# Kernel optimization log

Measured on AMD Instinct MI355X. Metric: run time of the kernel, lower is better.

Reference implementation:

```python
import jax, jax.numpy as jnp
import numpy as np

HIDDEN = 2048
N_HEADS = 16
N_KV = 4
HEAD_DIM = 128
SEQ = 2048
BATCH = 2
THETA = 10000.0


def rotate_half(x):
    half = x.shape[-1] // 2
    x1, x2 = x[..., :half], x[..., half:]
    return jnp.concatenate((-x2, x1), axis=-1)


def rope_cos_sin(seq_len, dim, theta, dtype):
    inv_freq = 1.0 / (theta ** (jnp.arange(0, dim, 2, dtype=jnp.float32) / dim))
    t = jnp.arange(seq_len, dtype=jnp.float32)
    freqs = jnp.einsum('i,j->ij', t, inv_freq)            # [S, dim/2]
    emb = jnp.concatenate((freqs, freqs), axis=-1)        # [S, dim]
    return jnp.cos(emb).astype(dtype), jnp.sin(emb).astype(dtype)


def setup_inputs() -> dict:
    key = jax.random.key(0)
    kx, kq, kk, kv, ko = jax.random.split(key, 5)
    s = 0.02
    return {
        'x':  jax.random.normal(kx, (BATCH, SEQ, HIDDEN), dtype=jnp.float32),
        'Wq': jax.random.normal(kq, (HIDDEN, N_HEADS * HEAD_DIM), dtype=jnp.float32) * s,
        'Wk': jax.random.normal(kk, (HIDDEN, N_KV * HEAD_DIM), dtype=jnp.float32) * s,
        'Wv': jax.random.normal(kv, (HIDDEN, N_KV * HEAD_DIM), dtype=jnp.float32) * s,
        'Wo': jax.random.normal(ko, (N_HEADS * HEAD_DIM, HIDDEN), dtype=jnp.float32) * s,
    }


def reference(x, Wq, Wk, Wv, Wo):
    B, S, _ = x.shape
    q = (x @ Wq).reshape(B, S, N_HEADS, HEAD_DIM)
    k = (x @ Wk).reshape(B, S, N_KV, HEAD_DIM)
    v = (x @ Wv).reshape(B, S, N_KV, HEAD_DIM)

    cos, sin = rope_cos_sin(S, HEAD_DIM, THETA, x.dtype)
    cos = cos[None, :, None, :]  # [1,S,1,D]
    sin = sin[None, :, None, :]
    q = q * cos + rotate_half(q) * sin
    k = k * cos + rotate_half(k) * sin

    repeat = N_HEADS // N_KV
    k = jnp.repeat(k, repeat, axis=2)  # repeat_interleave over heads
    v = jnp.repeat(v, repeat, axis=2)

    # [B,H,S,D]
    q = q.transpose(0, 2, 1, 3)
    k = k.transpose(0, 2, 1, 3)
    v = v.transpose(0, 2, 1, 3)

    scale = HEAD_DIM ** -0.5
    scores = jnp.einsum('bhqd,bhkd->bhqk', q, k) * scale
    causal = jnp.triu(jnp.full((S, S), -jnp.inf, dtype=scores.dtype), k=1)
    scores = scores + causal
    probs = jax.nn.softmax(scores, axis=-1)
    out = jnp.einsum('bhqk,bhkd->bhqd', probs, v)
    out = out.transpose(0, 2, 1, 3).reshape(B, S, N_HEADS * HEAD_DIM)
    return out @ Wo
```

## Files before the change

kernel.cpp:

```cpp
#include <hip/hip_runtime.h>
#include <hip/hip_bf16.h>
#include <math.h>

#define HIDDEN 2048
#define NHEADS 16
#define NKV 4
#define HD 128
#define SEQ 2048
#define BATCH 2
#define MTOT (BATCH*SEQ)
#define NQ (NHEADS*HD)
#define NKVD (NKV*HD)
#define NQKV (NQ + 2*NKVD)

typedef __attribute__((ext_vector_type(8))) short short8;
typedef __attribute__((ext_vector_type(4))) float float4v;

#if __has_builtin(__builtin_amdgcn_exp2f)
#define EXP2F __builtin_amdgcn_exp2f
#else
#define EXP2F exp2f
#endif
#define C1 0.1275174f

static __device__ __forceinline__ unsigned short f2bf(float f) {
  union { float f; unsigned int u; } v; v.f = f;
  unsigned int r = v.u + 0x7FFF + ((v.u >> 16) & 1);
  return (unsigned short)(r >> 16);
}
static __device__ __forceinline__ float bf2f(unsigned short h) {
  union { unsigned int u; float f; } v; v.u = ((unsigned int)h) << 16;
  return v.f;
}

static __device__ __forceinline__ void async16(const unsigned short* g, unsigned short* l) {
  __builtin_amdgcn_global_load_lds(
      (const __attribute__((address_space(1))) unsigned int*)g,
      (__attribute__((address_space(3))) unsigned int*)l, 16, 0, 0);
}

__global__ void cast_f32_bf16(const float* __restrict__ in,
                              unsigned short* __restrict__ out, int n) {
  int i = (blockIdx.x * blockDim.x + threadIdx.x) * 4;
  if (i < n) {
    float4 v = *(const float4*)(in + i);
    ushort4 o;
    o.x = f2bf(v.x); o.y = f2bf(v.y); o.z = f2bf(v.z); o.w = f2bf(v.w);
    *(ushort4*)(out + i) = o;
  }
}

__global__ void transpose_cast(const float* __restrict__ W,
                               unsigned short* __restrict__ Wt, int K, int N) {
  __shared__ float tile[32][33];
  int tn = blockIdx.x * 32;
  int tk = blockIdx.y * 32;
  int tx = threadIdx.x & 31;
  int ty = threadIdx.x >> 5;
  #pragma unroll
  for (int i = 0; i < 4; i++) {
    int k = tk + ty + i * 8;
    tile[ty + i * 8][tx] = W[(size_t)k * N + tn + tx];
  }
  __syncthreads();
  #pragma unroll
  for (int i = 0; i < 4; i++) {
    int n = tn + ty + i * 8;
    Wt[(size_t)n * K + tk + tx] = f2bf(tile[tx][ty + i * 8]);
  }
}

__global__ void rope_kernel(unsigned short* __restrict__ Qb, int nheads) {
  int idx = blockIdx.x * blockDim.x + threadIdx.x;
  int d = idx & 63;
  int hr = idx >> 6;
  int spos = (hr / nheads) % SEQ;
  size_t base = (size_t)hr * HD;
  float inv = exp2f((float)d * -0.2076205059304601f);
  float ang = (float)spos * inv;
  float sn, cs;
  sincosf(ang, &sn, &cs);
  float q1 = bf2f(Qb[base + d]);
  float q2 = bf2f(Qb[base + d + 64]);
  Qb[base + d]      = f2bf(q1 * cs - q2 * sn);
  Qb[base + d + 64] = f2bf(q2 * cs + q1 * sn);
}

__global__ __launch_bounds__(512, 2) void gemm_qkv(
    const unsigned short* __restrict__ A,
    const unsigned short* __restrict__ Bt,
    unsigned short* __restrict__ Qb,
    unsigned short* __restrict__ Kb,
    unsigned short* __restrict__ Vt) {
  __shared__ __align__(16) unsigned short L[4 * 16384];
  const int K = HIDDEN;
  const int NT = K / 32;
  int bm = blockIdx.y * 256, bn = blockIdx.x * 256;
  int tid = threadIdx.x, w = tid >> 6, lane = tid & 63;
  int wrow = w >> 2, wcol = w & 3;
  int m16 = lane & 15, quad = lane >> 4;
  int lrow = lane >> 2, lch = lane & 3;
  int lchs = lch ^ ((lrow >> 1) & 3);
  int qx = quad ^ ((m16 >> 1) & 3);
  const unsigned short* Ag = A + (size_t)(bm + w * 32 + lrow) * K + lchs * 8;
  const unsigned short* Bg = Bt + (size_t)(bn + w * 32 + lrow) * K + lchs * 8;

  float4v acc[8][4];
  #pragma unroll
  for (int i = 0; i < 8; i++)
    #pragma unroll
    for (int j = 0; j < 4; j++) acc[i][j] = (float4v)0.0f;

  auto stage = [&](int t) {
    unsigned short* Lb = L + (t & 3) * 16384;
    int k0 = t * 32;
    #pragma unroll
    for (int i = 0; i < 2; i++) {
      async16(Ag + (size_t)i * 16 * K + k0, Lb + w * 1024 + i * 512);
      async16(Bg + (size_t)i * 16 * K + k0, Lb + 8192 + w * 1024 + i * 512);
    }
  };

  const bool isV = (blockIdx.x >= 10);

  stage(0); stage(1);
  asm volatile("s_waitcnt vmcnt(4)" ::: "memory");
  __builtin_amdgcn_s_barrier();
  __builtin_amdgcn_sched_barrier(0);

  if (!isV) {
    for (int t = 0; t < NT; ++t) {
      if (t + 2 < NT) stage(t + 2);
      const unsigned short* Ab_ = L + (t & 3) * 16384;
      const unsigned short* Bb_ = Ab_ + 8192;
      short8 af[8], bfr[4];
      #pragma unroll
      for (int i = 0; i < 8; i++)
        af[i] = *(const short8*)(&Ab_[(wrow * 128 + i * 16 + m16) * 32 + qx * 8]);
      #pragma unroll
      for (int j = 0; j < 4; j++)
        bfr[j] = *(const short8*)(&Bb_[(wcol * 64 + j * 16 + m16) * 32 + qx * 8]);
      __builtin_amdgcn_s_setprio(1);
      #pragma unroll
      for (int i = 0; i < 8; i++)
        #pragma unroll
        for (int j = 0; j < 4; j++)
          acc[i][j] = __builtin_amdgcn_mfma_f32_16x16x32_bf16(af[i], bfr[j], acc[i][j], 0, 0, 0);
      __builtin_amdgcn_s_setprio(0);
      if (t + 2 < NT) { asm volatile("s_waitcnt vmcnt(4)" ::: "memory"); }
      else            { asm volatile("s_waitcnt vmcnt(0)" ::: "memory"); }
      __builtin_amdgcn_s_barrier();
      __builtin_amdgcn_sched_barrier(0);
    }
  } else {
    for (int t = 0; t < NT; ++t) {
      if (t + 2 < NT) stage(t + 2);
      const unsigned short* Ab_ = L + (t & 3) * 16384;
      const unsigned short* Bb_ = Ab_ + 8192;
      short8 af[8], bfr[4];
      #pragma unroll
      for (int i = 0; i < 8; i++)
        af[i] = *(const short8*)(&Ab_[(wrow * 128 + i * 16 + m16) * 32 + qx * 8]);
      #pragma unroll
      for (int j = 0; j < 4; j++)
        bfr[j] = *(const short8*)(&Bb_[(wcol * 64 + j * 16 + m16) * 32 + qx * 8]);
      __builtin_amdgcn_s_setprio(1);
      #pragma unroll
      for (int i = 0; i < 8; i++)
        #pragma unroll
        for (int j = 0; j < 4; j++)
          acc[i][j] = __builtin_amdgcn_mfma_f32_16x16x32_bf16(bfr[j], af[i], acc[i][j], 0, 0, 0);
      __builtin_amdgcn_s_setprio(0);
      if (t + 2 < NT) { asm volatile("s_waitcnt vmcnt(4)" ::: "memory"); }
      else            { asm volatile("s_waitcnt vmcnt(0)" ::: "memory"); }
      __builtin_amdgcn_s_barrier();
      __builtin_amdgcn_sched_barrier(0);
    }
  }

  if (blockIdx.x < 8) {
    #pragma unroll
    for (int i = 0; i < 8; i++)
      #pragma unroll
      for (int j = 0; j < 4; j++)
        #pragma unroll
        for (int r = 0; r < 4; r++) {
          int row = bm + wrow * 128 + i * 16 + quad * 4 + r;
          int col = bn + wcol * 64 + j * 16 + m16;
          Qb[(size_t)row * NQ + col] = f2bf(acc[i][j][r]);
        }
  } else if (!isV) {
    #pragma unroll
    for (int i = 0; i < 8; i++)
      #pragma unroll
      for (int j = 0; j < 4; j++)
        #pragma unroll
        for (int r = 0; r < 4; r++) {
          int row = bm + wrow * 128 + i * 16 + quad * 4 + r;
          int col = bn - 2048 + wcol * 64 + j * 16 + m16;
          Kb[(size_t)row * NKVD + col] = f2bf(acc[i][j][r]);
        }
  } else {
    #pragma unroll
    for (int i = 0; i < 8; i++)
      #pragma unroll
      for (int j = 0; j < 4; j++)
        #pragma unroll
        for (int r = 0; r < 4; r++) {
          int f = bn - 2560 + wcol * 64 + j * 16 + quad * 4 + r;
          int m = bm + wrow * 128 + i * 16 + m16;
          Vt[(size_t)f * MTOT + m] = f2bf(acc[i][j][r]);
        }
  }
}

__global__ __launch_bounds__(256) void gemm_o(
    const unsigned short* __restrict__ A,
    const unsigned short* __restrict__ Bt,
    float* __restrict__ C, int M, int N, int K) {
  __shared__ unsigned short As0[128 * 32], Bs0[128 * 32];
  __shared__ unsigned short As1[128 * 32], Bs1[128 * 32];
  int bm = blockIdx.y * 128, bn = blockIdx.x * 128;
  int tid = threadIdx.x, w = tid >> 6, lane = tid & 63;
  int wm = (w >> 1) * 64, wn = (w & 1) * 64;
  int m16 = lane & 15, quad = lane >> 4;
  int lrow = lane >> 2, lch = lane & 3;
  int lchs = lch ^ ((lrow >> 1) & 3);
  int qx = quad ^ ((m16 >> 1) & 3);
  const unsigned short* Ag = A + (size_t)(bm + w * 32 + lrow) * K + lchs * 8;
  const unsigned short* Bg = Bt + (size_t)(bn + w * 32 + lrow) * K + lchs * 8;
  int woff = w * 1024;

  float4v acc[4][4];
  #pragma unroll
  for (int i = 0; i < 4; i++)
    #pragma unroll
    for (int j = 0; j < 4; j++) acc[i][j] = (float4v)0.0f;

  auto stage = [&](int k0, unsigned short* Asl, unsigned short* Bsl) {
    #pragma unroll
    for (int i = 0; i < 2; i++) {
      async16(Ag + (size_t)i * 16 * K + k0, Asl + woff + i * 512);
      async16(Bg + (size_t)i * 16 * K + k0, Bsl + woff + i * 512);
    }
  };
  auto compute = [&](const unsigned short* As, const unsigned short* Bs) {
    short8 af[4], bfr[4];
    #pragma unroll
    for (int i = 0; i < 4; i++)
      af[i] = *(const short8*)(&As[(wm + i * 16 + m16) * 32 + qx * 8]);
    #pragma unroll
    for (int j = 0; j < 4; j++)
      bfr[j] = *(const short8*)(&Bs[(wn + j * 16 + m16) * 32 + qx * 8]);
    #pragma unroll
    for (int i = 0; i < 4; i++)
      #pragma unroll
      for (int j = 0; j < 4; j++)
        acc[i][j] = __builtin_amdgcn_mfma_f32_16x16x32_bf16(af[i], bfr[j], acc[i][j], 0, 0, 0);
  };

  stage(0, As0, Bs0);
  for (int k0 = 0; k0 < K; k0 += 64) {
    __syncthreads();
    if (k0 + 32 < K) stage(k0 + 32, As1, Bs1);
    compute(As0, Bs0);
    __syncthreads();
    if (k0 + 64 < K) stage(k0 + 64, As0, Bs0);
    compute(As1, Bs1);
  }

  #pragma unroll
  for (int i = 0; i < 4; i++)
    #pragma unroll
    for (int j = 0; j < 4; j++)
      #pragma unroll
      for (int r = 0; r < 4; r++) {
        int row = bm + wm + i * 16 + quad * 4 + r;
        int col = bn + wn + j * 16 + m16;
        C[(size_t)row * N + col] = acc[i][j][r];
      }
}

#define FLASH_TILE(CUR, NXT)                                                  \
  {                                                                           \
    const int ktb = kt * 64;                                                  \
    __syncthreads();        \
    {                                                                         \
      const unsigned short* Vg = Vt + vgrow * (size_t)MTOT                    \
                                    + (size_t)b * SEQ + ktb + kcv * 32 + vlch * 8; \
      unsigned short* Vl = Vs + kcv * 4096 + ipv * 512;                       \
      _Pragma("unroll")                                                       \
      for (int i = 0; i < 4; i++) async16(Vg + (size_t)i * 16 * MTOT, Vl + i * 512); \
    }                                                                         \
    if (kt < H) {                                                             \
      const unsigned short* Kg = Kp + (((size_t)b * SEQ + (kt + 1) * 64 + lrow) * NKV + kvh) * HD + w * 32 + vlch * 8; \
      unsigned short* Kl = NXT + w * 2048;                                    \
      _Pragma("unroll")                                                       \
      for (int i = 0; i < 4; i++) async16(Kg + (size_t)i * 16 * NKV * HD, Kl + i * 512); \
    }                                                                         \
    const bool act1 = (ktb <= lmax_w);                                        \
    float4v sacc[2][4];                                                       \
    _Pragma("unroll") for (int s4 = 0; s4 < 4; s4++) {                        \
      sacc[0][s4] = (float4v)0.0f; sacc[1][s4] = (float4v)0.0f; }             \
    __builtin_amdgcn_s_setprio(1);                                            \
    if (act1) {                                                               \
      _Pragma("unroll")                                                       \
      for (int s4 = 0; s4 < 4; s4++)                                          \
        _Pragma("unroll")                                                     \
        for (int c = 0; c < 4; c++) {                                         \
          short8 kf = *(const short8*)(&CUR[c * 2048 + (s4 * 16 + m16) * 32 + qx * 8]); \
          sacc[0][s4] = __builtin_amdgcn_mfma_f32_16x16x32_bf16(kf, qf[0][c], sacc[0][s4], 0, 0, 0); \
          sacc[1][s4] = __builtin_amdgcn_mfma_f32_16x16x32_bf16(kf, qf[1][c], sacc[1][s4], 0, 0, 0); \
        }                                                                     \
    } else {                                                                  \
      _Pragma("unroll")                                                       \
      for (int s4 = 0; s4 < 4; s4++)                                          \
        _Pragma("unroll")                                                     \
        for (int c = 0; c < 4; c++) {                                         \
          short8 kf = *(const short8*)(&CUR[c * 2048 + (s4 * 16 + m16) * 32 + qx * 8]); \
          sacc[0][s4] = __builtin_amdgcn_mfma_f32_16x16x32_bf16(kf, qf[0][c], sacc[0][s4], 0, 0, 0); \
        }                                                                     \
    }                                                                         \
    __builtin_amdgcn_s_setprio(0);                                            \
    _Pragma("unroll")                                                         \
    for (int qs = 0; qs < 2; qs++) {                                          \
      if (qs == 0 || act1) {                                                  \
        const int tb = qs ? L : H;                                            \
        const int qabs = tb * 64 + w * 16 + m16;                              \
        const bool diag = (kt == tb);                                         \
        float sv[4][4]; float mloc = -1e30f;                                  \
        if (diag) {                                                           \
          _Pragma("unroll") for (int s4 = 0; s4 < 4; s4++)                    \
            _Pragma("unroll") for (int r = 0; r < 4; r++) {                   \
              int kabs = ktb + s4 * 16 + quad * 4 + r;                        \
              float t = sacc[qs][s4][r];                                      \
              sv[s4][r] = (kabs > qabs) ? -1e30f : t;                         \
              mloc = fmaxf(mloc, sv[s4][r]); }                                \
        } else {                                                              \
          _Pragma("unroll") for (int s4 = 0; s4 < 4; s4++)                    \
            _Pragma("unroll") for (int r = 0; r < 4; r++) {                   \
              sv[s4][r] = sacc[qs][s4][r]; mloc = fmaxf(mloc, sv[s4][r]); }   \
        }                                                                     \
        mloc *= C1;                                                           \
        mloc = fmaxf(mloc, __shfl_xor(mloc, 16, 64));                         \
        mloc = fmaxf(mloc, __shfl_xor(mloc, 32, 64));                         \
        float mnewS = fmaxf(miS[qs], mloc);                                   \
        const bool defer = (bool)__all(mloc <= miS[qs] + 8.0f);               \
        if (defer) mnewS = miS[qs];  \
        const int prow = qs * 64 + w * 16 + m16;                              \
        const int psw = prow * 32; const int rx = prow & 7;                   \
        float rs = 0.0f;                                                      \
        _Pragma("unroll") for (int s4 = 0; s4 < 4; s4++) {                    \
          float p0 = EXP2F(__builtin_fmaf(sv[s4][0], C1, -mnewS));            \
          float p1 = EXP2F(__builtin_fmaf(sv[s4][1], C1, -mnewS));            \
          float p2 = EXP2F(__builtin_fmaf(sv[s4][2], C1, -mnewS));            \
          float p3 = EXP2F(__builtin_fmaf(sv[s4][3], C1, -mnewS));            \
          rs += p0 + p1 + p2 + p3;                                            \
          uint2 u;                                                            \
          u.x = (__float_as_uint(p1) & 0xffff0000u) | (__float_as_uint(p0) >> 16); \
          u.y = (__float_as_uint(p3) & 0xffff0000u) | (__float_as_uint(p2) >> 16); \
          int chunkW = s4 * 2 + (quad >> 1);                                  \
          *(uint2*)(&Ps[psw + ((chunkW ^ rx) << 2) + (quad & 1) * 2]) = u;    \
        }                                                                     \
        rs += __shfl_xor(rs, 16, 64);                                         \
        rs += __shfl_xor(rs, 32, 64);                                         \
        if (!defer) {                                                         \
          const float alpha = EXP2F(miS[qs] - mnewS);                         \
          li[qs] *= alpha; miS[qs] = mnewS;                                   \
          _Pragma("unroll") for (int ds = 0; ds < 8; ds++) oacc[ds][qs] *= alpha; \
        }                                                                     \
        li[qs] += rs;                                                         \
      }                                                                       \
    }                                                                         \
    __syncthreads();     \
    {                                                                         \
      const int r0 = w * 16 + m16, r1 = 64 + w * 16 + m16;                    \
      __builtin_amdgcn_s_setprio(1);                                          \
      if (act1) {                                                             \
        _Pragma("unroll")                                                     \
        for (int kc = 0; kc < 2; kc++) {                                      \
          short8 pf0 = *(const short8*)(&Ps[r0 * 32 + (((kc * 4 + quad) ^ (r0 & 7)) << 2)]); \
          short8 pf1 = *(const short8*)(&Ps[r1 * 32 + (((kc * 4 + quad) ^ (r1 & 7)) << 2)]); \
          _Pragma("unroll")                                                   \
          for (int ds = 0; ds < 8; ds++) {                                    \
            short8 vf = *(const short8*)(&Vs[kc * 4096 + (ds * 16 + m16) * 32 + qx * 8]); \
            oacc[ds][0] = __builtin_amdgcn_mfma_f32_16x16x32_bf16(vf, pf0, oacc[ds][0], 0, 0, 0); \
            oacc[ds][1] = __builtin_amdgcn_mfma_f32_16x16x32_bf16(vf, pf1, oacc[ds][1], 0, 0, 0); \
          }                                                                   \
        }                                                                     \
      } else {                                                                \
        _Pragma("unroll")                                                     \
        for (int kc = 0; kc < 2; kc++) {                                      \
          short8 pf0 = *(const short8*)(&Ps[r0 * 32 + (((kc * 4 + quad) ^ (r0 & 7)) << 2)]); \
          _Pragma("unroll")                                                   \
          for (int ds = 0; ds < 8; ds++) {                                    \
            short8 vf = *(const short8*)(&Vs[kc * 4096 + (ds * 16 + m16) * 32 + qx * 8]); \
            oacc[ds][0] = __builtin_amdgcn_mfma_f32_16x16x32_bf16(vf, pf0, oacc[ds][0], 0, 0, 0); \
          }                                                                   \
        }                                                                     \
      }                                                                       \
      __builtin_amdgcn_s_setprio(0);                                          \
    }                                                                         \
  }

__global__ __launch_bounds__(256, 2) void flash_attn(
    const unsigned short* __restrict__ Q,
    const unsigned short* __restrict__ Kp,
    const unsigned short* __restrict__ Vt,
    unsigned short* __restrict__ O) {
  __shared__ unsigned short Ks0[4 * 64 * 32];
  __shared__ unsigned short Ks1[4 * 64 * 32];
  __shared__ unsigned short Vs[2 * 128 * 32];
  __shared__ unsigned int   Ps[128 * 32];

  int bx = blockIdx.x;
  int h  = blockIdx.y;
  int b  = blockIdx.z;
  int kvh = h >> 2;
  int H = 31 - bx, L = bx;
  int tid = threadIdx.x;
  int w = tid >> 6, lane = tid & 63;
  int m16 = lane & 15, quad = lane >> 4;
  int lrow = lane >> 2, lch = lane & 3;
  const int vlch = lch ^ ((lrow >> 1) & 3);
  const int qx = quad ^ ((m16 >> 1) & 3);
  const int lmax_w = L * 64 + w * 16 + 15;

  const int kcv = w >> 1, ipv = (w & 1) * 4;
  const size_t vgrow = (size_t)kvh * HD + ipv * 16 + lrow;

  short8 qf[2][4];
  #pragma unroll
  for (int qs = 0; qs < 2; qs++) {
    int tb = qs ? L : H;
    size_t qbase = (((size_t)b * SEQ + tb * 64 + w * 16 + m16) * NHEADS + h) * HD;
    #pragma unroll
    for (int c = 0; c < 4; c++)
      qf[qs][c] = *(const short8*)(Q + qbase + c * 32 + quad * 8);
  }

  float4v oacc[8][2];
  #pragma unroll
  for (int ds = 0; ds < 8; ds++) { oacc[ds][0] = (float4v)0.0f; oacc[ds][1] = (float4v)0.0f; }
  float miS[2] = {-1e30f, -1e30f}, li[2] = {0.0f, 0.0f};

  {
    const unsigned short* Kg = Kp + (((size_t)b * SEQ + lrow) * NKV + kvh) * HD + w * 32 + vlch * 8;
    unsigned short* Kl = Ks0 + w * 2048;
    #pragma unroll
    for (int i = 0; i < 4; i++) async16(Kg + (size_t)i * 16 * NKV * HD, Kl + i * 512);
  }

  int kt = 0;
  for (;;) {
    FLASH_TILE(Ks0, Ks1)
    if (++kt > H) break;
    FLASH_TILE(Ks1, Ks0)
    if (++kt > H) break;
  }

  #pragma unroll
  for (int qs = 0; qs < 2; qs++) {
    float inv = 1.0f / li[qs];
    int tb = qs ? L : H;
    int qabs = tb * 64 + w * 16 + m16;
    size_t obase = (((size_t)b * SEQ + qabs) * NHEADS + h) * HD + quad * 4;
    #pragma unroll
    for (int ds = 0; ds < 8; ds++) {
      float v0 = oacc[ds][qs][0] * inv;
      float v1 = oacc[ds][qs][1] * inv;
      float v2 = oacc[ds][qs][2] * inv;
      float v3 = oacc[ds][qs][3] * inv;
      uint2 u;
      u.x = ((unsigned)f2bf(v1) << 16) | f2bf(v0);
      u.y = ((unsigned)f2bf(v3) << 16) | f2bf(v2);
      *(uint2*)(O + obase + ds * 16) = u;
    }
  }
}

extern "C" void kernel_launch(void* const* d_in, const int* in_sizes, int n_in,
                              void* d_out, int out_size, void* d_ws, size_t ws_size,
                              hipStream_t stream) {
  const float* x  = (const float*)d_in[0];
  const float* Wq = (const float*)d_in[1];
  const float* Wk = (const float*)d_in[2];
  const float* Wv = (const float*)d_in[3];
  const float* Wo = (const float*)d_in[4];
  float* out = (float*)d_out;

  unsigned short* ws = (unsigned short*)d_ws;
  unsigned short* xb  = ws;
  unsigned short* Wqt = xb  + (size_t)MTOT * HIDDEN;
  unsigned short* Wkt = Wqt + (size_t)NQ * HIDDEN;
  unsigned short* Wvt = Wkt + (size_t)NKVD * HIDDEN;
  unsigned short* Wot = Wvt + (size_t)NKVD * HIDDEN;
  unsigned short* Qb  = Wot + (size_t)NQ * HIDDEN;
  unsigned short* Kb  = Qb  + (size_t)MTOT * NQ;
  unsigned short* Vtb = Kb  + (size_t)MTOT * NKVD;
  unsigned short* Ab  = Vtb + (size_t)MTOT * NKVD;

  cast_f32_bf16<<<(MTOT * HIDDEN / 4 + 255) / 256, 256, 0, stream>>>(x, xb, MTOT * HIDDEN);
  transpose_cast<<<dim3(NQ / 32, HIDDEN / 32), 256, 0, stream>>>(Wq, Wqt, HIDDEN, NQ);
  transpose_cast<<<dim3(NKVD / 32, HIDDEN / 32), 256, 0, stream>>>(Wk, Wkt, HIDDEN, NKVD);
  transpose_cast<<<dim3(NKVD / 32, HIDDEN / 32), 256, 0, stream>>>(Wv, Wvt, HIDDEN, NKVD);
  transpose_cast<<<dim3(NQ / 32, HIDDEN / 32), 256, 0, stream>>>(Wo, Wot, NQ, HIDDEN);

  gemm_qkv<<<dim3(NQKV / 256, MTOT / 256), 512, 0, stream>>>(xb, Wqt, Qb, Kb, Vtb);

  rope_kernel<<<(BATCH * SEQ * NHEADS * 64) / 256, 256, 0, stream>>>(Qb, NHEADS);
  rope_kernel<<<(BATCH * SEQ * NKV * 64) / 256, 256, 0, stream>>>(Kb, NKV);

  flash_attn<<<dim3(16, NHEADS, BATCH), 256, 0, stream>>>(Qb, Kb, Vtb, Ab);

  gemm_o<<<dim3(HIDDEN / 128, MTOT / 128), 256, 0, stream>>>(Ab, Wot, out, MTOT, HIDDEN, NQ);
}
```

Baseline: 300.3 us.

## Deepen GEMM prefetch to three stages and double-buffer V tiles in flash attention

```diff
diff --git a/kernel.cpp b/kernel.cpp
--- a/kernel.cpp
+++ b/kernel.cpp
@@ -123,14 +123,14 @@
 
   const bool isV = (blockIdx.x >= 10);
 
-  stage(0); stage(1);
-  asm volatile("s_waitcnt vmcnt(4)" ::: "memory");
+  stage(0); stage(1); stage(2);
+  asm volatile("s_waitcnt vmcnt(8)" ::: "memory");
   __builtin_amdgcn_s_barrier();
   __builtin_amdgcn_sched_barrier(0);
 
   if (!isV) {
     for (int t = 0; t < NT; ++t) {
-      if (t + 2 < NT) stage(t + 2);
+      if (t + 3 < NT) stage(t + 3);
       const unsigned short* Ab_ = L + (t & 3) * 16384;
       const unsigned short* Bb_ = Ab_ + 8192;
       short8 af[8], bfr[4];
@@ -147,14 +147,15 @@
         for (int j = 0; j < 4; j++)
           acc[i][j] = __builtin_amdgcn_mfma_f32_16x16x32_bf16(af[i], bfr[j], acc[i][j], 0, 0, 0);
       __builtin_amdgcn_s_setprio(0);
-      if (t + 2 < NT) { asm volatile("s_waitcnt vmcnt(4)" ::: "memory"); }
-      else            { asm volatile("s_waitcnt vmcnt(0)" ::: "memory"); }
+      if (t + 3 < NT)      { asm volatile("s_waitcnt vmcnt(8)" ::: "memory"); }
+      else if (t + 2 < NT) { asm volatile("s_waitcnt vmcnt(4)" ::: "memory"); }
+      else                 { asm volatile("s_waitcnt vmcnt(0)" ::: "memory"); }
       __builtin_amdgcn_s_barrier();
       __builtin_amdgcn_sched_barrier(0);
     }
   } else {
     for (int t = 0; t < NT; ++t) {
-      if (t + 2 < NT) stage(t + 2);
+      if (t + 3 < NT) stage(t + 3);
       const unsigned short* Ab_ = L + (t & 3) * 16384;
       const unsigned short* Bb_ = Ab_ + 8192;
       short8 af[8], bfr[4];
@@ -171,8 +172,9 @@
         for (int j = 0; j < 4; j++)
           acc[i][j] = __builtin_amdgcn_mfma_f32_16x16x32_bf16(bfr[j], af[i], acc[i][j], 0, 0, 0);
       __builtin_amdgcn_s_setprio(0);
-      if (t + 2 < NT) { asm volatile("s_waitcnt vmcnt(4)" ::: "memory"); }
-      else            { asm volatile("s_waitcnt vmcnt(0)" ::: "memory"); }
+      if (t + 3 < NT)      { asm volatile("s_waitcnt vmcnt(8)" ::: "memory"); }
+      else if (t + 2 < NT) { asm volatile("s_waitcnt vmcnt(4)" ::: "memory"); }
+      else                 { asm volatile("s_waitcnt vmcnt(0)" ::: "memory"); }
       __builtin_amdgcn_s_barrier();
       __builtin_amdgcn_sched_barrier(0);
     }
@@ -281,23 +283,28 @@
       }
 }
 
-#define FLASH_TILE(CUR, NXT)                                                  \
+#define FLASH_TILE(CUR, NXT, PC, PN)                                          \
   {                                                                           \
     const int ktb = kt * 64;                                                  \
-    __syncthreads();        \
-    {                                                                         \
+    asm volatile("s_waitcnt lgkmcnt(0)" ::: "memory");                        \
+    __builtin_amdgcn_s_barrier();             \
+    __builtin_amdgcn_sched_barrier(0);                                        \
+    if (kt < H) {                                                             \
       const unsigned short* Vg = Vt + vgrow * (size_t)MTOT                    \
-                                    + (size_t)b * SEQ + ktb + kcv * 32 + vlch * 8; \
-      unsigned short* Vl = Vs + kcv * 4096 + ipv * 512;                       \
+                                    + (size_t)b * SEQ + (ktb + 64) + kcv * 32 + vlch * 8; \
+      unsigned short* Vl = Vs + (PN) * 8192 + kcv * 4096 + ipv * 512;         \
       _Pragma("unroll")                                                       \
       for (int i = 0; i < 4; i++) async16(Vg + (size_t)i * 16 * MTOT, Vl + i * 512); \
-    }                                                                         \
-    if (kt < H) {                                                             \
       const unsigned short* Kg = Kp + (((size_t)b * SEQ + (kt + 1) * 64 + lrow) * NKV + kvh) * HD + w * 32 + vlch * 8; \
       unsigned short* Kl = NXT + w * 2048;                                    \
       _Pragma("unroll")                                                       \
       for (int i = 0; i < 4; i++) async16(Kg + (size_t)i * 16 * NKV * HD, Kl + i * 512); \
+      asm volatile("s_waitcnt vmcnt(8)" ::: "memory");                        \
+    } else {                                                                  \
+      asm volatile("s_waitcnt vmcnt(0)" ::: "memory");                        \
     }                                                                         \
+    __builtin_amdgcn_s_barrier();       \
+    __builtin_amdgcn_sched_barrier(0);                                        \
     const bool act1 = (ktb <= lmax_w);                                        \
     float4v sacc[2][4];                                                       \
     _Pragma("unroll") for (int s4 = 0; s4 < 4; s4++) {                        \
@@ -372,7 +379,8 @@
         li[qs] += rs;                                                         \
       }                                                                       \
     }                                                                         \
-    __syncthreads();     \
+    asm volatile("s_waitcnt lgkmcnt(0)" ::: "memory");  \
+    __builtin_amdgcn_sched_barrier(0);                                        \
     {                                                                         \
       const int r0 = w * 16 + m16, r1 = 64 + w * 16 + m16;                    \
       __builtin_amdgcn_s_setprio(1);                                          \
@@ -383,7 +391,7 @@
           short8 pf1 = *(const short8*)(&Ps[r1 * 32 + (((kc * 4 + quad) ^ (r1 & 7)) << 2)]); \
           _Pragma("unroll")                                                   \
           for (int ds = 0; ds < 8; ds++) {                                    \
-            short8 vf = *(const short8*)(&Vs[kc * 4096 + (ds * 16 + m16) * 32 + qx * 8]); \
+            short8 vf = *(const short8*)(&Vs[(PC) * 8192 + kc * 4096 + (ds * 16 + m16) * 32 + qx * 8]); \
             oacc[ds][0] = __builtin_amdgcn_mfma_f32_16x16x32_bf16(vf, pf0, oacc[ds][0], 0, 0, 0); \
             oacc[ds][1] = __builtin_amdgcn_mfma_f32_16x16x32_bf16(vf, pf1, oacc[ds][1], 0, 0, 0); \
           }                                                                   \
@@ -394,7 +402,7 @@
           short8 pf0 = *(const short8*)(&Ps[r0 * 32 + (((kc * 4 + quad) ^ (r0 & 7)) << 2)]); \
           _Pragma("unroll")                                                   \
           for (int ds = 0; ds < 8; ds++) {                                    \
-            short8 vf = *(const short8*)(&Vs[kc * 4096 + (ds * 16 + m16) * 32 + qx * 8]); \
+            short8 vf = *(const short8*)(&Vs[(PC) * 8192 + kc * 4096 + (ds * 16 + m16) * 32 + qx * 8]); \
             oacc[ds][0] = __builtin_amdgcn_mfma_f32_16x16x32_bf16(vf, pf0, oacc[ds][0], 0, 0, 0); \
           }                                                                   \
         }                                                                     \
@@ -410,7 +418,7 @@
     unsigned short* __restrict__ O) {
   __shared__ unsigned short Ks0[4 * 64 * 32];
   __shared__ unsigned short Ks1[4 * 64 * 32];
-  __shared__ unsigned short Vs[2 * 128 * 32];
+  __shared__ unsigned short Vs[2 * 2 * 128 * 32];
   __shared__ unsigned int   Ps[128 * 32];
 
   int bx = blockIdx.x;
@@ -445,6 +453,10 @@
   float miS[2] = {-1e30f, -1e30f}, li[2] = {0.0f, 0.0f};
 
   {
+    const unsigned short* Vg = Vt + vgrow * (size_t)MTOT + (size_t)b * SEQ + kcv * 32 + vlch * 8;
+    unsigned short* Vl = Vs + kcv * 4096 + ipv * 512;
+    #pragma unroll
+    for (int i = 0; i < 4; i++) async16(Vg + (size_t)i * 16 * MTOT, Vl + i * 512);
     const unsigned short* Kg = Kp + (((size_t)b * SEQ + lrow) * NKV + kvh) * HD + w * 32 + vlch * 8;
     unsigned short* Kl = Ks0 + w * 2048;
     #pragma unroll
@@ -453,9 +465,9 @@
 
   int kt = 0;
   for (;;) {
-    FLASH_TILE(Ks0, Ks1)
+    FLASH_TILE(Ks0, Ks1, 0, 1)
     if (++kt > H) break;
-    FLASH_TILE(Ks1, Ks0)
+    FLASH_TILE(Ks1, Ks0, 1, 0)
     if (++kt > H) break;
   }
 
```

New measurement: 295.7 us. Within noise of the previous version (-1.5%).

## Single-buffer K/V tiles to raise flash-attention occupancy to three blocks per CU

Applied to the files above, without the earlier changes.

```diff
diff --git a/kernel.cpp b/kernel.cpp
--- a/kernel.cpp
+++ b/kernel.cpp
@@ -281,23 +281,12 @@
       }
 }
 
-#define FLASH_TILE(CUR, NXT)                                                  \
+#define FLASH_TILE()                                                          \
   {                                                                           \
     const int ktb = kt * 64;                                                  \
-    __syncthreads();        \
-    {                                                                         \
-      const unsigned short* Vg = Vt + vgrow * (size_t)MTOT                    \
-                                    + (size_t)b * SEQ + ktb + kcv * 32 + vlch * 8; \
-      unsigned short* Vl = Vs + kcv * 4096 + ipv * 512;                       \
-      _Pragma("unroll")                                                       \
-      for (int i = 0; i < 4; i++) async16(Vg + (size_t)i * 16 * MTOT, Vl + i * 512); \
-    }                                                                         \
-    if (kt < H) {                                                             \
-      const unsigned short* Kg = Kp + (((size_t)b * SEQ + (kt + 1) * 64 + lrow) * NKV + kvh) * HD + w * 32 + vlch * 8; \
-      unsigned short* Kl = NXT + w * 2048;                                    \
-      _Pragma("unroll")                                                       \
-      for (int i = 0; i < 4; i++) async16(Kg + (size_t)i * 16 * NKV * HD, Kl + i * 512); \
-    }                                                                         \
+    asm volatile("s_waitcnt vmcnt(0)" ::: "memory");                          \
+    __builtin_amdgcn_s_barrier();       \
+    __builtin_amdgcn_sched_barrier(0);                                        \
     const bool act1 = (ktb <= lmax_w);                                        \
     float4v sacc[2][4];                                                       \
     _Pragma("unroll") for (int s4 = 0; s4 < 4; s4++) {                        \
@@ -308,7 +297,7 @@
       for (int s4 = 0; s4 < 4; s4++)                                          \
         _Pragma("unroll")                                                     \
         for (int c = 0; c < 4; c++) {                                         \
-          short8 kf = *(const short8*)(&CUR[c * 2048 + (s4 * 16 + m16) * 32 + qx * 8]); \
+          short8 kf = *(const short8*)(&Ks[c * 2048 + (s4 * 16 + m16) * 32 + qx * 8]); \
           sacc[0][s4] = __builtin_amdgcn_mfma_f32_16x16x32_bf16(kf, qf[0][c], sacc[0][s4], 0, 0, 0); \
           sacc[1][s4] = __builtin_amdgcn_mfma_f32_16x16x32_bf16(kf, qf[1][c], sacc[1][s4], 0, 0, 0); \
         }                                                                     \
@@ -317,7 +306,7 @@
       for (int s4 = 0; s4 < 4; s4++)                                          \
         _Pragma("unroll")                                                     \
         for (int c = 0; c < 4; c++) {                                         \
-          short8 kf = *(const short8*)(&CUR[c * 2048 + (s4 * 16 + m16) * 32 + qx * 8]); \
+          short8 kf = *(const short8*)(&Ks[c * 2048 + (s4 * 16 + m16) * 32 + qx * 8]); \
           sacc[0][s4] = __builtin_amdgcn_mfma_f32_16x16x32_bf16(kf, qf[0][c], sacc[0][s4], 0, 0, 0); \
         }                                                                     \
     }                                                                         \
@@ -372,7 +361,8 @@
         li[qs] += rs;                                                         \
       }                                                                       \
     }                                                                         \
-    __syncthreads();     \
+    asm volatile("s_waitcnt lgkmcnt(0)" ::: "memory");  \
+    __builtin_amdgcn_sched_barrier(0);                                        \
     {                                                                         \
       const int r0 = w * 16 + m16, r1 = 64 + w * 16 + m16;                    \
       __builtin_amdgcn_s_setprio(1);                                          \
@@ -401,15 +391,28 @@
       }                                                                       \
       __builtin_amdgcn_s_setprio(0);                                          \
     }                                                                         \
-  }
-
-__global__ __launch_bounds__(256, 2) void flash_attn(
+    asm volatile("s_waitcnt lgkmcnt(0)" ::: "memory");  \
+    __builtin_amdgcn_s_barrier();             \
+    __builtin_amdgcn_sched_barrier(0);                                        \
+    if (kt < H) {                                                             \
+      const unsigned short* Vg = Vt + vgrow * (size_t)MTOT                    \
+                                    + (size_t)b * SEQ + (ktb + 64) + kcv * 32 + vlch * 8; \
+      unsigned short* Vl = Vs + kcv * 4096 + ipv * 512;                       \
+      _Pragma("unroll")                                                       \
+      for (int i = 0; i < 4; i++) async16(Vg + (size_t)i * 16 * MTOT, Vl + i * 512); \
+      const unsigned short* Kg = Kp + (((size_t)b * SEQ + (kt + 1) * 64 + lrow) * NKV + kvh) * HD + w * 32 + vlch * 8; \
+      unsigned short* Kl = Ks + w * 2048;                                     \
+      _Pragma("unroll")                                                       \
+      for (int i = 0; i < 4; i++) async16(Kg + (size_t)i * 16 * NKV * HD, Kl + i * 512); \
+    }                                                                         \
+  }
+
+__global__ __launch_bounds__(256, 3) void flash_attn(
     const unsigned short* __restrict__ Q,
     const unsigned short* __restrict__ Kp,
     const unsigned short* __restrict__ Vt,
     unsigned short* __restrict__ O) {
-  __shared__ unsigned short Ks0[4 * 64 * 32];
-  __shared__ unsigned short Ks1[4 * 64 * 32];
+  __shared__ unsigned short Ks[4 * 64 * 32];
   __shared__ unsigned short Vs[2 * 128 * 32];
   __shared__ unsigned int   Ps[128 * 32];
 
@@ -445,18 +448,18 @@
   float miS[2] = {-1e30f, -1e30f}, li[2] = {0.0f, 0.0f};
 
   {
+    const unsigned short* Vg = Vt + vgrow * (size_t)MTOT + (size_t)b * SEQ + kcv * 32 + vlch * 8;
+    unsigned short* Vl = Vs + kcv * 4096 + ipv * 512;
+    #pragma unroll
+    for (int i = 0; i < 4; i++) async16(Vg + (size_t)i * 16 * MTOT, Vl + i * 512);
     const unsigned short* Kg = Kp + (((size_t)b * SEQ + lrow) * NKV + kvh) * HD + w * 32 + vlch * 8;
-    unsigned short* Kl = Ks0 + w * 2048;
+    unsigned short* Kl = Ks + w * 2048;
     #pragma unroll
     for (int i = 0; i < 4; i++) async16(Kg + (size_t)i * 16 * NKV * HD, Kl + i * 512);
   }
 
-  int kt = 0;
-  for (;;) {
-    FLASH_TILE(Ks0, Ks1)
-    if (++kt > H) break;
-    FLASH_TILE(Ks1, Ks0)
-    if (++kt > H) break;
+  for (int kt = 0; kt <= H; ++kt) {
+    FLASH_TILE()
   }
 
   #pragma unroll
```

Result: no change. 305.9 us (+1.9%).

## Merge weight transposes and RoPE launches; deepen O-projection GEMM prefetch pipeline

Applied to the files above, without the earlier changes.

```diff
diff --git a/kernel.cpp b/kernel.cpp
--- a/kernel.cpp
+++ b/kernel.cpp
@@ -50,10 +50,19 @@
   }
 }
 
-__global__ void transpose_cast(const float* __restrict__ W,
-                               unsigned short* __restrict__ Wt, int K, int N) {
+__global__ void transpose_cast_all(
+    const float* __restrict__ Wq, const float* __restrict__ Wk,
+    const float* __restrict__ Wv, const float* __restrict__ Wo,
+    unsigned short* __restrict__ Wqt, unsigned short* __restrict__ Wkt,
+    unsigned short* __restrict__ Wvt, unsigned short* __restrict__ Wot) {
   __shared__ float tile[32][33];
-  int tn = blockIdx.x * 32;
+  const int K = 2048;
+  int bx = blockIdx.x;
+  const float* W; unsigned short* Wt; int N; int tn;
+  if (bx < 64)      { W = Wq; Wt = Wqt; N = NQ;     tn = bx * 32; }
+  else if (bx < 80) { W = Wk; Wt = Wkt; N = NKVD;   tn = (bx - 64) * 32; }
+  else if (bx < 96) { W = Wv; Wt = Wvt; N = NKVD;   tn = (bx - 80) * 32; }
+  else              { W = Wo; Wt = Wot; N = HIDDEN; tn = (bx - 96) * 32; }
   int tk = blockIdx.y * 32;
   int tx = threadIdx.x & 31;
   int ty = threadIdx.x >> 5;
@@ -70,8 +79,13 @@
   }
 }
 
-__global__ void rope_kernel(unsigned short* __restrict__ Qb, int nheads) {
+__global__ void rope_all(unsigned short* __restrict__ Qb,
+                         unsigned short* __restrict__ Kb) {
   int idx = blockIdx.x * blockDim.x + threadIdx.x;
+  const int QTOT = MTOT * NHEADS * 64;
+  unsigned short* P; int nheads;
+  if (idx < QTOT) { P = Qb; nheads = NHEADS; }
+  else            { P = Kb; nheads = NKV; idx -= QTOT; }
   int d = idx & 63;
   int hr = idx >> 6;
   int spos = (hr / nheads) % SEQ;
@@ -80,10 +94,10 @@
   float ang = (float)spos * inv;
   float sn, cs;
   sincosf(ang, &sn, &cs);
-  float q1 = bf2f(Qb[base + d]);
-  float q2 = bf2f(Qb[base + d + 64]);
-  Qb[base + d]      = f2bf(q1 * cs - q2 * sn);
-  Qb[base + d + 64] = f2bf(q2 * cs + q1 * sn);
+  float q1 = bf2f(P[base + d]);
+  float q2 = bf2f(P[base + d + 64]);
+  P[base + d]      = f2bf(q1 * cs - q2 * sn);
+  P[base + d + 64] = f2bf(q2 * cs + q1 * sn);
 }
 
 __global__ __launch_bounds__(512, 2) void gemm_qkv(
@@ -214,12 +228,12 @@
   }
 }
 
-__global__ __launch_bounds__(256) void gemm_o(
+__global__ __launch_bounds__(256, 2) void gemm_o(
     const unsigned short* __restrict__ A,
     const unsigned short* __restrict__ Bt,
     float* __restrict__ C, int M, int N, int K) {
-  __shared__ unsigned short As0[128 * 32], Bs0[128 * 32];
-  __shared__ unsigned short As1[128 * 32], Bs1[128 * 32];
+  __shared__ __align__(16) unsigned short L[4 * 8192];
+  const int NT = K / 32;
   int bm = blockIdx.y * 128, bn = blockIdx.x * 128;
   int tid = threadIdx.x, w = tid >> 6, lane = tid & 63;
   int wm = (w >> 1) * 64, wn = (w & 1) * 64;
@@ -229,7 +243,6 @@
   int qx = quad ^ ((m16 >> 1) & 3);
   const unsigned short* Ag = A + (size_t)(bm + w * 32 + lrow) * K + lchs * 8;
   const unsigned short* Bg = Bt + (size_t)(bn + w * 32 + lrow) * K + lchs * 8;
-  int woff = w * 1024;
 
   float4v acc[4][4];
   #pragma unroll
@@ -237,36 +250,43 @@
     #pragma unroll
     for (int j = 0; j < 4; j++) acc[i][j] = (float4v)0.0f;
 
-  auto stage = [&](int k0, unsigned short* Asl, unsigned short* Bsl) {
+  auto stage = [&](int t) {
+    unsigned short* Lb = L + (t & 3) * 8192;
+    int k0 = t * 32;
     #pragma unroll
     for (int i = 0; i < 2; i++) {
-      async16(Ag + (size_t)i * 16 * K + k0, Asl + woff + i * 512);
-      async16(Bg + (size_t)i * 16 * K + k0, Bsl + woff + i * 512);
+      async16(Ag + (size_t)i * 16 * K + k0, Lb + w * 1024 + i * 512);
+      async16(Bg + (size_t)i * 16 * K + k0, Lb + 4096 + w * 1024 + i * 512);
     }
   };
-  auto compute = [&](const unsigned short* As, const unsigned short* Bs) {
+
+  stage(0); stage(1);
+  asm volatile("s_waitcnt vmcnt(4)" ::: "memory");
+  __builtin_amdgcn_s_barrier();
+  __builtin_amdgcn_sched_barrier(0);
+
+  for (int t = 0; t < NT; ++t) {
+    if (t + 2 < NT) stage(t + 2);
+    const unsigned short* Ab_ = L + (t & 3) * 8192;
+    const unsigned short* Bb_ = Ab_ + 4096;
     short8 af[4], bfr[4];
     #pragma unroll
     for (int i = 0; i < 4; i++)
-      af[i] = *(const short8*)(&As[(wm + i * 16 + m16) * 32 + qx * 8]);
+      af[i] = *(const short8*)(&Ab_[(wm + i * 16 + m16) * 32 + qx * 8]);
     #pragma unroll
     for (int j = 0; j < 4; j++)
-      bfr[j] = *(const short8*)(&Bs[(wn + j * 16 + m16) * 32 + qx * 8]);
+      bfr[j] = *(const short8*)(&Bb_[(wn + j * 16 + m16) * 32 + qx * 8]);
+    __builtin_amdgcn_s_setprio(1);
     #pragma unroll
     for (int i = 0; i < 4; i++)
       #pragma unroll
       for (int j = 0; j < 4; j++)
         acc[i][j] = __builtin_amdgcn_mfma_f32_16x16x32_bf16(af[i], bfr[j], acc[i][j], 0, 0, 0);
-  };
-
-  stage(0, As0, Bs0);
-  for (int k0 = 0; k0 < K; k0 += 64) {
-    __syncthreads();
-    if (k0 + 32 < K) stage(k0 + 32, As1, Bs1);
-    compute(As0, Bs0);
-    __syncthreads();
-    if (k0 + 64 < K) stage(k0 + 64, As0, Bs0);
-    compute(As1, Bs1);
+    __builtin_amdgcn_s_setprio(0);
+    if (t + 2 < NT) { asm volatile("s_waitcnt vmcnt(4)" ::: "memory"); }
+    else            { asm volatile("s_waitcnt vmcnt(0)" ::: "memory"); }
+    __builtin_amdgcn_s_barrier();
+    __builtin_amdgcn_sched_barrier(0);
   }
 
   #pragma unroll
@@ -501,15 +521,11 @@
   unsigned short* Ab  = Vtb + (size_t)MTOT * NKVD;
 
   cast_f32_bf16<<<(MTOT * HIDDEN / 4 + 255) / 256, 256, 0, stream>>>(x, xb, MTOT * HIDDEN);
-  transpose_cast<<<dim3(NQ / 32, HIDDEN / 32), 256, 0, stream>>>(Wq, Wqt, HIDDEN, NQ);
-  transpose_cast<<<dim3(NKVD / 32, HIDDEN / 32), 256, 0, stream>>>(Wk, Wkt, HIDDEN, NKVD);
-  transpose_cast<<<dim3(NKVD / 32, HIDDEN / 32), 256, 0, stream>>>(Wv, Wvt, HIDDEN, NKVD);
-  transpose_cast<<<dim3(NQ / 32, HIDDEN / 32), 256, 0, stream>>>(Wo, Wot, NQ, HIDDEN);
+  transpose_cast_all<<<dim3(160, 64), 256, 0, stream>>>(Wq, Wk, Wv, Wo, Wqt, Wkt, Wvt, Wot);
 
   gemm_qkv<<<dim3(NQKV / 256, MTOT / 256), 512, 0, stream>>>(xb, Wqt, Qb, Kb, Vtb);
 
-  rope_kernel<<<(BATCH * SEQ * NHEADS * 64) / 256, 256, 0, stream>>>(Qb, NHEADS);
-  rope_kernel<<<(BATCH * SEQ * NKV * 64) / 256, 256, 0, stream>>>(Kb, NKV);
+  rope_all<<<(MTOT * (NHEADS + NKV) * 64) / 256, 256, 0, stream>>>(Qb, Kb);
 
   flash_attn<<<dim3(16, NHEADS, BATCH), 256, 0, stream>>>(Qb, Kb, Vtb, Ab);
 
```

Result: faster. 286.3 us (-4.7%).
